# Kernel optimization log

Measured on AMD Instinct MI355X. Metric: run time of the kernel, lower is better.

The kernel has to match this reference:

```python
import jax, jax.numpy as jnp
import numpy as np

EPS_INTERP = 1e-8
EPS_BN = 1e-5


def _bn_relu(x, gamma, beta):
    # x: [B, C, N]; training-mode BatchNorm1d over (B, N) with biased variance
    mean = jnp.mean(x, axis=(0, 2), keepdims=True)
    var = jnp.mean((x - mean) ** 2, axis=(0, 2), keepdims=True)
    xn = (x - mean) / jnp.sqrt(var + EPS_BN)
    return jax.nn.relu(xn * gamma[None, :, None] + beta[None, :, None])


def setup_inputs() -> dict:
    key = jax.random.key(0)
    ks = jax.random.split(key, 8)
    B, N, S, D = 16, 4096, 1024, 128
    return {
        "xyz1": jax.random.normal(ks[0], (B, 3, N), jnp.float32),
        "xyz2": jax.random.normal(ks[1], (B, 3, S), jnp.float32),
        "points1": jax.random.normal(ks[2], (B, D, N), jnp.float32),
        "points2": jax.random.normal(ks[3], (B, D, S), jnp.float32),
        "w0": jax.random.normal(ks[4], (256, 512), jnp.float32) * 0.04,
        "b0": jax.random.normal(ks[5], (256,), jnp.float32) * 0.01,
        "gamma0": jnp.ones((256,), jnp.float32),
        "beta0": jnp.zeros((256,), jnp.float32),
        "w1": jax.random.normal(ks[6], (128, 256), jnp.float32) * 0.06,
        "b1": jax.random.normal(ks[7], (128,), jnp.float32) * 0.01,
        "gamma1": jnp.ones((128,), jnp.float32),
        "beta1": jnp.zeros((128,), jnp.float32),
    }


def reference(xyz1, xyz2, points1, points2, w0, b0, gamma0, beta0, w1, b1, gamma1, beta1):
    # to [B, N, C] layouts
    x1 = jnp.transpose(xyz1, (0, 2, 1))   # [B, N, 3]
    x2 = jnp.transpose(xyz2, (0, 2, 1))   # [B, S, 3]
    p2 = jnp.transpose(points2, (0, 2, 1))  # [B, S, D]
    B, N, _ = x1.shape

    # squared pairwise distances [B, N, S]
    dists = (jnp.sum(x1 ** 2, -1)[:, :, None]
             + jnp.sum(x2 ** 2, -1)[:, None, :]
             - 2.0 * jnp.einsum('bnc,bsc->bns', x1, x2))

    # 3 nearest neighbors (ascending distance)
    neg_d, idx = jax.lax.top_k(-dists, 3)   # idx: [B, N, 3]
    d3 = -neg_d
    recip = 1.0 / (d3 + EPS_INTERP)
    weight = recip / jnp.sum(recip, axis=2, keepdims=True)  # [B, N, 3]

    # gather neighbor features: [B, N, 3, D]
    gathered = jax.vmap(lambda p, i: p[i])(p2, idx)
    # NOTE: this repo flattens the 3 weighted neighbors (no sum) -> [B, N, 3*D]
    interp = (gathered * weight[..., None]).reshape(B, N, -1)

    new_pts = jnp.concatenate([jnp.transpose(points1, (0, 2, 1)), interp], axis=-1)  # [B, N, 512]
    x = jnp.transpose(new_pts, (0, 2, 1))  # [B, 512, N]

    x = _bn_relu(jnp.einsum('oc,bcn->bon', w0, x) + b0[None, :, None], gamma0, beta0)
    x = _bn_relu(jnp.einsum('oc,bcn->bon', w1, x) + b1[None, :, None], gamma1, beta1)
    return x
```

## Files before the change

kernel.cpp:

```cpp
#include <hip/hip_runtime.h>
#include <stdint.h>

typedef unsigned short ushort_t;
typedef __attribute__((ext_vector_type(8))) __bf16 bf16x8;
typedef __attribute__((ext_vector_type(4))) float f32x4;

__device__ __forceinline__ float b2f(ushort_t u) {
    unsigned v = ((unsigned)u) << 16;
    float f;
    __builtin_memcpy(&f, &v, 4);
    return f;
}

__device__ __forceinline__ ushort_t f2b(float f) {
    __bf16 h = (__bf16)f;
    return __builtin_bit_cast(ushort_t, h);
}

__device__ __forceinline__ void gl_lds16(const void* g, void* l) {
    __builtin_amdgcn_global_load_lds((const __attribute__((address_space(1))) void*)g,
                                     (__attribute__((address_space(3))) void*)l, 16, 0, 0);
}

__global__ __launch_bounds__(256) void k_pre(const float* __restrict__ w0, ushort_t* __restrict__ w0b,
                                             const float* __restrict__ w1, ushort_t* __restrict__ w1b,
                                             const float* __restrict__ xyz2, float4* __restrict__ sdat,
                                             const float* __restrict__ points2, ushort_t* __restrict__ p2t,
                                             float* __restrict__ zb) {
    int bid = blockIdx.x;
    int t = threadIdx.x;
    if (bid < 512) {
        int i = bid * 256 + t;
        w0b[i] = f2b(w0[i]);
    } else if (bid < 640) {
        int i = (bid - 512) * 256 + t;
        w1b[i] = f2b(w1[i]);
    } else if (bid < 704) {
        int bb = bid - 640;
        int b = bb & 15, by = bb >> 4;
        int s = by * 256 + t;
        const float* x2 = xyz2 + (size_t)b * 3 * 1024;
        float x = x2[s], y = x2[1024 + s], z = x2[2048 + s];
        float4 v;
        v.x = x; v.y = y; v.z = z;
        v.w = __fadd_rn(__fadd_rn(__fmul_rn(x, x), __fmul_rn(y, y)), __fmul_rn(z, z));
        sdat[(size_t)b * 1024 + s] = v;
    } else if (bid < 960) {
        int bb = bid - 704;
        int b = bb & 15, sy = bb >> 4;
        int s = sy * 64 + (t & 63);
        int g = t >> 6;
        const float* src = points2 + (size_t)b * 128 * 1024 + s;
        ushort_t* dst = p2t + ((size_t)b * 1024 + s) * 128;
#pragma unroll
        for (int i = 0; i < 4; ++i) {
            int cp = i * 4 + g;
            ushort_t tmp[8];
#pragma unroll
            for (int k = 0; k < 8; ++k) tmp[k] = f2b(src[(size_t)(cp * 8 + k) * 1024]);
            *(uint4*)(dst + cp * 8) = *(const uint4*)tmp;
        }
    } else {
        for (int i = t; i < 6144; i += 256) zb[i] = 0.f;
    }
}

__global__ __launch_bounds__(256) void k_interp(const float* __restrict__ xyz1,
                                                const float4* __restrict__ sdat,
                                                const float* __restrict__ points1,
                                                const ushort_t* __restrict__ p2t,
                                                ushort_t* __restrict__ X) {
    int b = blockIdx.x;
    int n0 = blockIdx.y * 32;
    int t = threadIdx.x;
    int tq = t & 31;
    int slice = t >> 5;
    int wave = t >> 6, lane = t & 63;

    __shared__ __align__(16) char sbuf[16384];
    float4* sP = (float4*)sbuf;
    int*   sidx = (int*)sbuf;
    float* sw   = (float*)(sbuf + 384);
    __shared__ float sD[768];
    __shared__ int   sI[768];

    {
        const float4* src = sdat + (size_t)b * 1024;
#pragma unroll
        for (int c = 0; c < 4; ++c) {
            int p = wave * 256 + c * 64 + lane;
            gl_lds16(src + p, sbuf + p * 16);
        }
    }

    int n = n0 + tq;
    float x = xyz1[((size_t)b * 3 + 0) * 4096 + n];
    float y = xyz1[((size_t)b * 3 + 1) * 4096 + n];
    float z = xyz1[((size_t)b * 3 + 2) * 4096 + n];
    float s1 = __fadd_rn(__fadd_rn(__fmul_rn(x, x), __fmul_rn(y, y)), __fmul_rn(z, z));

    __syncthreads();

    const float* p1base = points1 + (size_t)b * 128 * 4096 + n0 + tq;
    float p1v[16];
#pragma unroll
    for (int i = 0; i < 2; ++i)
#pragma unroll
        for (int k = 0; k < 8; ++k)
            p1v[i * 8 + k] = p1base[(size_t)(((i * 8 + slice) * 8) + k) * 4096];

    float d0 = 1e30f, d1 = 1e30f, d2 = 1e30f;
    int i0 = 0, i1 = 0, i2 = 0;
    int sbeg = slice * 128;
    const float4* sdL = sP + sbeg;
#pragma unroll 8
    for (int s = 0; s < 128; ++s) {
        float4 v = sdL[s];
        float dot = fmaf(z, v.z, fmaf(y, v.y, __fmul_rn(x, v.x)));
        float d = __fadd_rn(fmaf(-2.0f, dot, s1), v.w);
        int si = sbeg + s;
        bool c0 = d < d0, c1 = d < d1, c2 = d < d2;
        i2 = c1 ? i1 : (c2 ? si : i2);
        i1 = c0 ? i0 : (c1 ? si : i1);
        i0 = c0 ? si : i0;
        d2 = fminf(fmaxf(d, d1), d2);
        d1 = fminf(fmaxf(d, d0), d1);
        d0 = fminf(d, d0);
    }
    sD[t * 3 + 0] = d0; sD[t * 3 + 1] = d1; sD[t * 3 + 2] = d2;
    sI[t * 3 + 0] = i0; sI[t * 3 + 1] = i1; sI[t * 3 + 2] = i2;

    {
        ushort_t* dstbase = X + (size_t)(b * 4096 + n0 + tq) * 512;
#pragma unroll
        for (int i = 0; i < 2; ++i) {
            int piece = i * 8 + slice;
            ushort_t tmp[8];
#pragma unroll
            for (int k = 0; k < 8; ++k) tmp[k] = f2b(p1v[i * 8 + k]);
            *(uint4*)(dstbase + piece * 8) = *(const uint4*)tmp;
        }
    }
    __syncthreads();

    if (t < 32) {
        int sel0 = -1, sel1 = -1;
        float seld[3]; int seli[3];
#pragma unroll
        for (int r = 0; r < 3; ++r) {
            float bd = 1e38f; int bi = 1 << 30;
            for (int k = 0; k < 24; ++k) {
                int s3 = (k * 0xAAAB) >> 17;
                int rank = k - s3 * 3;
                int base = (s3 * 32 + t) * 3 + rank;
                float cd = sD[base];
                int ci = sI[base];
                bool excl = (ci == sel0) | (ci == sel1);
                bool better = (!excl) & ((cd < bd) | ((cd == bd) & (ci < bi)));
                if (better) { bd = cd; bi = ci; }
            }
            seld[r] = bd; seli[r] = bi;
            if (r == 0) sel0 = bi; else if (r == 1) sel1 = bi;
        }
        float r0 = 1.0f / (seld[0] + 1e-8f);
        float r1 = 1.0f / (seld[1] + 1e-8f);
        float r2 = 1.0f / (seld[2] + 1e-8f);
        float rs = r0 + r1 + r2;
        sw[t * 3 + 0] = r0 / rs; sw[t * 3 + 1] = r1 / rs; sw[t * 3 + 2] = r2 / rs;
        sidx[t * 3 + 0] = seli[0]; sidx[t * 3 + 1] = seli[1]; sidx[t * 3 + 2] = seli[2];
    }
    __syncthreads();

#pragma unroll
    for (int i = 0; i < 6; ++i) {
        int idx = i * 256 + t;
        int q = idx / 48;
        int rem = idx - q * 48;
        int r = rem >> 4;
        int piece = rem & 15;
        int si = sidx[q * 3 + r] & 1023;
        float wt = sw[q * 3 + r];
        const ushort_t* src = p2t + ((size_t)b * 1024 + si) * 128 + piece * 8;
        uint4 raw = *(const uint4*)src;
        ushort_t* e = (ushort_t*)&raw;
        ushort_t outv[8];
#pragma unroll
        for (int k = 0; k < 8; ++k) outv[k] = f2b(wt * b2f(e[k]));
        ushort_t* dst = X + (size_t)(b * 4096 + n0 + q) * 512 + 128 + r * 128 + piece * 8;
        *(uint4*)dst = *(const uint4*)outv;
    }
}

__global__ __launch_bounds__(512, 4) void k_gemm(const ushort_t* __restrict__ A,
                                                 const ushort_t* __restrict__ Bt,
                                                 const float* __restrict__ bias,
                                                 ushort_t* __restrict__ Y,
                                                 float* __restrict__ gs,
                                                 float* __restrict__ gq,
                                                 int Mtot, int K) {
    __shared__ __align__(16) char smem[51200];
    ushort_t* As = (ushort_t*)smem;
    ushort_t* Bs = (ushort_t*)(smem + 32768);
    ushort_t* sY = (ushort_t*)smem;
    float* red_s = (float*)(smem + 49152);
    float* red_q = red_s + 256;

    int t = threadIdx.x;
    int j0 = blockIdx.x * 128;
    int wave = t >> 6, lane = t & 63;
    int wm = wave >> 1, wn = wave & 1;
    int l16 = lane & 15, quad = lane >> 4;

    if (t < 256) { red_s[t] = 0.f; red_q[t] = 0.f; }

    f32x4 acc[4][4] = {};

    int nk = K >> 6;
    for (int kt = 0; kt < nk; ++kt) {
#pragma unroll
        for (int c = 0; c < 4; ++c) {
            int idx = c * 512 + t;
            int row = idx >> 3, kc = idx & 7;
            gl_lds16(A + (size_t)row * K + kt * 64 + kc * 8, As + idx * 8);
        }
#pragma unroll
        for (int c = 0; c < 2; ++c) {
            int idx = c * 512 + t;
            int row = idx >> 3, kc = idx & 7;
            gl_lds16(Bt + (size_t)(j0 + row) * K + kt * 64 + kc * 8, Bs + idx * 8);
        }
        __syncthreads();

#pragma unroll
        for (int kk = 0; kk < 2; ++kk) {
            bf16x8 af[4], bfr[4];
#pragma unroll
            for (int mi = 0; mi < 4; ++mi)
                af[mi] = *(const bf16x8*)(As + (wm * 64 + mi * 16 + l16) * 64 + kk * 32 + quad * 8);
#pragma unroll
            for (int ni = 0; ni < 4; ++ni)
                bfr[ni] = *(const bf16x8*)(Bs + (wn * 64 + ni * 16 + l16) * 64 + kk * 32 + quad * 8);
#pragma unroll
            for (int mi = 0; mi < 4; ++mi)
#pragma unroll
                for (int ni = 0; ni < 4; ++ni)
                    acc[mi][ni] = __builtin_amdgcn_mfma_f32_16x16x32_bf16(af[mi], bfr[ni], acc[mi][ni], 0, 0, 0);
        }
        __syncthreads();
    }

#pragma unroll
    for (int h = 0; h < 2; ++h) {
        if ((wm >> 1) == h) {
#pragma unroll
            for (int mi = 0; mi < 4; ++mi) {
                int obase = wm * 64 + mi * 16 + quad * 4;
                int ocol = obase - h * 128;
                float bv[4];
#pragma unroll
                for (int r = 0; r < 4; ++r) bv[r] = bias[obase + r];
                float sr[4] = {0.f, 0.f, 0.f, 0.f}, qr[4] = {0.f, 0.f, 0.f, 0.f};
#pragma unroll
                for (int ni = 0; ni < 4; ++ni) {
                    int j_local = wn * 64 + ni * 16 + l16;
                    ushort4 pk;
                    float v0 = acc[mi][ni][0] + bv[0];
                    float v1 = acc[mi][ni][1] + bv[1];
                    float v2 = acc[mi][ni][2] + bv[2];
                    float v3 = acc[mi][ni][3] + bv[3];
                    pk.x = f2b(v0); pk.y = f2b(v1); pk.z = f2b(v2); pk.w = f2b(v3);
                    sr[0] += v0; qr[0] += v0 * v0;
                    sr[1] += v1; qr[1] += v1 * v1;
                    sr[2] += v2; qr[2] += v2 * v2;
                    sr[3] += v3; qr[3] += v3 * v3;
                    *(ushort4*)(sY + j_local * 136 + ocol) = pk;
                }
#pragma unroll
                for (int r = 0; r < 4; ++r) {
                    float s = sr[r], q = qr[r];
                    s += __shfl_xor(s, 1); s += __shfl_xor(s, 2);
                    s += __shfl_xor(s, 4); s += __shfl_xor(s, 8);
                    q += __shfl_xor(q, 1); q += __shfl_xor(q, 2);
                    q += __shfl_xor(q, 4); q += __shfl_xor(q, 8);
                    if (l16 == 0) {
                        atomicAdd(&red_s[obase + r], s);
                        atomicAdd(&red_q[obase + r], q);
                    }
                }
            }
        }
        __syncthreads();
#pragma unroll
        for (int rep = 0; rep < 4; ++rep) {
            int idx = rep * 512 + t;
            int jl = idx >> 4;
            int o8 = idx & 15;
            uint4 vv = *(const uint4*)(sY + jl * 136 + o8 * 8);
            *(uint4*)(Y + (size_t)(j0 + jl) * Mtot + h * 128 + o8 * 8) = vv;
        }
        __syncthreads();
    }
    if (t < 256) {
        int cp = blockIdx.x & 7;
        atomicAdd(&gs[cp * 256 + t], red_s[t]);
        atomicAdd(&gq[cp * 256 + t], red_q[t]);
    }
}

__global__ __launch_bounds__(256) void k_gemmf(const ushort_t* __restrict__ A,
                                               const ushort_t* __restrict__ Y0,
                                               const float* __restrict__ bias,
                                               const float* __restrict__ gamma0,
                                               const float* __restrict__ beta0,
                                               const float* __restrict__ gs0,
                                               const float* __restrict__ gq0,
                                               ushort_t* __restrict__ Y,
                                               float* __restrict__ gs1,
                                               float* __restrict__ gq1,
                                               int Mtot, int K) {
    __shared__ __align__(16) char smem[35840];
    ushort_t* As = (ushort_t*)smem;
    ushort_t* Bs = (ushort_t*)(smem + 16384);
    float* sa = (float*)(smem + 32768);
    float* sb = (float*)(smem + 33792);
    ushort_t* sY = (ushort_t*)smem;
    float* red_s = (float*)(smem + 34816);
    float* red_q = red_s + 128;

    int t = threadIdx.x;
    int m0 = blockIdx.x * 128;
    int j0 = blockIdx.y * 128;
    int wave = t >> 6, lane = t & 63;
    int wm = wave >> 1, wn = wave & 1;
    int l16 = lane & 15, quad = lane >> 4;

    {
        float s = 0.f, q = 0.f;
#pragma unroll
        for (int k = 0; k < 8; ++k) { s += gs0[k * 256 + t]; q += gq0[k * 256 + t]; }
        float mean = s * (1.0f / 65536.0f);
        float var = q * (1.0f / 65536.0f) - mean * mean;
        float sc = gamma0[t] / sqrtf(var + 1e-5f);
        sa[t] = sc;
        sb[t] = beta0[t] - mean * sc;
    }
    if (t < 128) { red_s[t] = 0.f; red_q[t] = 0.f; }
    __syncthreads();

    f32x4 acc[4][4] = {};

    int nk = K >> 6;
    for (int kt = 0; kt < nk; ++kt) {
#pragma unroll
        for (int c = 0; c < 4; ++c) {
            int idx = c * 256 + t;
            int row = idx >> 3, kc = idx & 7;
            gl_lds16(A + (size_t)(m0 + row) * K + kt * 64 + kc * 8, As + idx * 8);
        }
#pragma unroll
        for (int c = 0; c < 4; ++c) {
            int idx = c * 256 + t;
            int row = idx >> 3, kc = idx & 7;
            int cbase = kt * 64 + kc * 8;
            uint4 raw = *(const uint4*)(Y0 + (size_t)(j0 + row) * K + cbase);
            ushort_t* e = (ushort_t*)&raw;
            ushort_t outv[8];
#pragma unroll
            for (int k = 0; k < 8; ++k) {
                float v = fmaxf(sa[cbase + k] * b2f(e[k]) + sb[cbase + k], 0.f);
                outv[k] = f2b(v);
            }
            *(uint4*)(Bs + idx * 8) = *(const uint4*)outv;
        }
        __syncthreads();

#pragma unroll
        for (int kk = 0; kk < 2; ++kk) {
            bf16x8 af[4], bfr[4];
#pragma unroll
            for (int mi = 0; mi < 4; ++mi)
                af[mi] = *(const bf16x8*)(As + (wm * 64 + mi * 16 + l16) * 64 + kk * 32 + quad * 8);
#pragma unroll
            for (int ni = 0; ni < 4; ++ni)
                bfr[ni] = *(const bf16x8*)(Bs + (wn * 64 + ni * 16 + l16) * 64 + kk * 32 + quad * 8);
#pragma unroll
            for (int mi = 0; mi < 4; ++mi)
#pragma unroll
                for (int ni = 0; ni < 4; ++ni)
                    acc[mi][ni] = __builtin_amdgcn_mfma_f32_16x16x32_bf16(af[mi], bfr[ni], acc[mi][ni], 0, 0, 0);
        }
        __syncthreads();
    }

#pragma unroll
    for (int mi = 0; mi < 4; ++mi) {
        int obase = wm * 64 + mi * 16 + quad * 4;
        float bv[4];
#pragma unroll
        for (int r = 0; r < 4; ++r) bv[r] = bias[m0 + obase + r];
        float sr[4] = {0.f, 0.f, 0.f, 0.f}, qr[4] = {0.f, 0.f, 0.f, 0.f};
#pragma unroll
        for (int ni = 0; ni < 4; ++ni) {
            int j_local = wn * 64 + ni * 16 + l16;
            ushort4 pk;
            float v0 = acc[mi][ni][0] + bv[0];
            float v1 = acc[mi][ni][1] + bv[1];
            float v2 = acc[mi][ni][2] + bv[2];
            float v3 = acc[mi][ni][3] + bv[3];
            pk.x = f2b(v0); pk.y = f2b(v1); pk.z = f2b(v2); pk.w = f2b(v3);
            sr[0] += v0; qr[0] += v0 * v0;
            sr[1] += v1; qr[1] += v1 * v1;
            sr[2] += v2; qr[2] += v2 * v2;
            sr[3] += v3; qr[3] += v3 * v3;
            *(ushort4*)(sY + j_local * 136 + obase) = pk;
        }
#pragma unroll
        for (int r = 0; r < 4; ++r) {
            float s = sr[r], q = qr[r];
            s += __shfl_xor(s, 1); s += __shfl_xor(s, 2);
            s += __shfl_xor(s, 4); s += __shfl_xor(s, 8);
            q += __shfl_xor(q, 1); q += __shfl_xor(q, 2);
            q += __shfl_xor(q, 4); q += __shfl_xor(q, 8);
            if (l16 == 0) {
                atomicAdd(&red_s[obase + r], s);
                atomicAdd(&red_q[obase + r], q);
            }
        }
    }
    __syncthreads();

#pragma unroll
    for (int rep = 0; rep < 8; ++rep) {
        int idx = rep * 256 + t;
        int jl = idx >> 4;
        int o8 = idx & 15;
        uint4 vv = *(const uint4*)(sY + jl * 136 + o8 * 8);
        *(uint4*)(Y + (size_t)(j0 + jl) * Mtot + m0 + o8 * 8) = vv;
    }
    if (t < 128) {
        int cp = blockIdx.y & 7;
        atomicAdd(&gs1[cp * 128 + m0 + t], red_s[t]);
        atomicAdd(&gq1[cp * 128 + m0 + t], red_q[t]);
    }
}

__global__ __launch_bounds__(256) void k_out(const ushort_t* __restrict__ Y1,
                                             const float* __restrict__ gs1,
                                             const float* __restrict__ gq1,
                                             const float* __restrict__ gamma1,
                                             const float* __restrict__ beta1,
                                             float* __restrict__ out) {
    __shared__ float sa[128], sb[128];
    int t = threadIdx.x;
    if (t < 128) {
        float s = 0.f, q = 0.f;
#pragma unroll
        for (int k = 0; k < 8; ++k) { s += gs1[k * 128 + t]; q += gq1[k * 128 + t]; }
        float mean = s * (1.0f / 65536.0f);
        float var = q * (1.0f / 65536.0f) - mean * mean;
        float sc = gamma1[t] / sqrtf(var + 1e-5f);
        sa[t] = sc;
        sb[t] = beta1[t] - mean * sc;
    }
    __syncthreads();
    int b = blockIdx.x;
    int nl = t & 127;
    int half = t >> 7;
    int n = blockIdx.y * 128 + nl;
    const uint4* src = (const uint4*)(Y1 + (size_t)(b * 4096 + n) * 128);
    float* dst = out + (size_t)b * 128 * 4096 + n;
    uint4 raw[8];
#pragma unroll
    for (int p = 0; p < 8; ++p) raw[p] = src[half * 8 + p];
    const ushort_t* e = (const ushort_t*)raw;
#pragma unroll
    for (int c = 0; c < 64; ++c) {
        int ch = half * 64 + c;
        float v = b2f(e[c]);
        v = fmaxf(sa[ch] * v + sb[ch], 0.f);
        dst[(size_t)ch * 4096] = v;
    }
}

extern "C" void kernel_launch(void* const* d_in, const int* in_sizes, int n_in,
                              void* d_out, int out_size, void* d_ws, size_t ws_size,
                              hipStream_t stream) {
    const float* xyz1    = (const float*)d_in[0];
    const float* xyz2    = (const float*)d_in[1];
    const float* points1 = (const float*)d_in[2];
    const float* points2 = (const float*)d_in[3];
    const float* w0      = (const float*)d_in[4];
    const float* b0      = (const float*)d_in[5];
    const float* gamma0  = (const float*)d_in[6];
    const float* beta0   = (const float*)d_in[7];
    const float* w1      = (const float*)d_in[8];
    const float* b1      = (const float*)d_in[9];
    const float* gamma1  = (const float*)d_in[10];
    const float* beta1   = (const float*)d_in[11];
    float* out = (float*)d_out;

    char* ws = (char*)d_ws;
    const size_t OFF_X    = 0;
    const size_t OFF_Y0   = 67108864;
    const size_t OFF_Y1   = 100663296;
    const size_t OFF_P2T  = 117440512;
    const size_t OFF_W0B  = 121634816;
    const size_t OFF_W1B  = 121896960;
    const size_t OFF_SDAT = 121965568;
    const size_t OFF_AB   = 122227712;

    ushort_t* X    = (ushort_t*)(ws + OFF_X);
    ushort_t* Y0   = (ushort_t*)(ws + OFF_Y0);
    ushort_t* Y1   = (ushort_t*)(ws + OFF_Y1);
    ushort_t* p2t  = (ushort_t*)(ws + OFF_P2T);
    ushort_t* w0b  = (ushort_t*)(ws + OFF_W0B);
    ushort_t* w1b  = (ushort_t*)(ws + OFF_W1B);
    float4* sdat   = (float4*)(ws + OFF_SDAT);
    float* ab      = (float*)(ws + OFF_AB);
    float* gs0 = ab;               float* gq0 = ab + 2048;
    float* gs1 = ab + 4096;        float* gq1 = ab + 5120;

    k_pre<<<961, 256, 0, stream>>>(w0, w0b, w1, w1b, xyz2, sdat, points2, p2t, ab);
    k_interp<<<dim3(16, 128), 256, 0, stream>>>(xyz1, sdat, points1, p2t, X);
    k_gemm<<<512, 512, 0, stream>>>(w0b, X, b0, Y0, gs0, gq0, 256, 512);
    k_gemmf<<<dim3(1, 512), 256, 0, stream>>>(w1b, Y0, b1, gamma0, beta0, gs0, gq0, Y1, gs1, gq1, 128, 256);
    k_out<<<dim3(16, 32), 256, 0, stream>>>(Y1, gs1, gq1, gamma1, beta1, out);
}
```

Measured before the change: 204.2 us.

## Fuse interpolation and first GEMM to keep concatenated features in LDS

The interpolation kernel now builds the 32x512 concatenated bf16 feature tile in shared memory with an XOR swizzle instead of writing it to a global X buffer. It then runs the first 256x512 projection on that tile directly with MFMA, reading the weights from global memory, and writes Y0 plus the BN partial sums. This drops the 64 MB X write and its re-read by a separate GEMM kernel, and one launch. In exchange each block reloads the full weight matrix from global/L2 with small 32-column tiles, shared memory doubles, and the per-block global atomics to the BN stats increase.

```diff
diff --git a/kernel.cpp b/kernel.cpp
--- a/kernel.cpp
+++ b/kernel.cpp
@@ -65,24 +65,31 @@
     }
 }
 
-__global__ __launch_bounds__(256) void k_interp(const float* __restrict__ xyz1,
-                                                const float4* __restrict__ sdat,
-                                                const float* __restrict__ points1,
-                                                const ushort_t* __restrict__ p2t,
-                                                ushort_t* __restrict__ X) {
+__global__ __launch_bounds__(256, 4) void k_fused(const float* __restrict__ xyz1,
+                                                  const float4* __restrict__ sdat,
+                                                  const float* __restrict__ points1,
+                                                  const ushort_t* __restrict__ p2t,
+                                                  const ushort_t* __restrict__ W,
+                                                  const float* __restrict__ bias,
+                                                  ushort_t* __restrict__ Y0,
+                                                  float* __restrict__ gs,
+                                                  float* __restrict__ gq) {
     int b = blockIdx.x;
     int n0 = blockIdx.y * 32;
     int t = threadIdx.x;
     int tq = t & 31;
     int slice = t >> 5;
     int wave = t >> 6, lane = t & 63;
-
-    __shared__ __align__(16) char sbuf[16384];
+    int l16 = lane & 15, quad = lane >> 4;
+
+    __shared__ __align__(16) char sbuf[32768];
     float4* sP = (float4*)sbuf;
-    int*   sidx = (int*)sbuf;
-    float* sw   = (float*)(sbuf + 384);
-    __shared__ float sD[768];
-    __shared__ int   sI[768];
+    float* sD  = (float*)(sbuf + 16384);
+    int*   sI  = (int*)(sbuf + 19456);
+    ushort_t* Xs  = (ushort_t*)sbuf;
+    ushort_t* sYl = (ushort_t*)sbuf;
+    __shared__ int   sidx[96];
+    __shared__ float sw[96];
 
     {
         const float4* src = sdat + (size_t)b * 1024;
@@ -129,18 +136,6 @@
     }
     sD[t * 3 + 0] = d0; sD[t * 3 + 1] = d1; sD[t * 3 + 2] = d2;
     sI[t * 3 + 0] = i0; sI[t * 3 + 1] = i1; sI[t * 3 + 2] = i2;
-
-    {
-        ushort_t* dstbase = X + (size_t)(b * 4096 + n0 + tq) * 512;
-#pragma unroll
-        for (int i = 0; i < 2; ++i) {
-            int piece = i * 8 + slice;
-            ushort_t tmp[8];
-#pragma unroll
-            for (int k = 0; k < 8; ++k) tmp[k] = f2b(p1v[i * 8 + k]);
-            *(uint4*)(dstbase + piece * 8) = *(const uint4*)tmp;
-        }
-    }
     __syncthreads();
 
     if (t < 32) {
@@ -171,6 +166,16 @@
     }
     __syncthreads();
 
+    {
+#pragma unroll
+        for (int i = 0; i < 2; ++i) {
+            int piece = i * 8 + slice;
+            ushort_t tmp[8];
+#pragma unroll
+            for (int k = 0; k < 8; ++k) tmp[k] = f2b(p1v[i * 8 + k]);
+            *(uint4*)(Xs + tq * 512 + ((piece ^ (tq & 7)) * 8)) = *(const uint4*)tmp;
+        }
+    }
 #pragma unroll
     for (int i = 0; i < 6; ++i) {
         int idx = i * 256 + t;
@@ -180,130 +185,79 @@
         int piece = rem & 15;
         int si = sidx[q * 3 + r] & 1023;
         float wt = sw[q * 3 + r];
-        const ushort_t* src = p2t + ((size_t)b * 1024 + si) * 128 + piece * 8;
-        uint4 raw = *(const uint4*)src;
+        uint4 raw = *(const uint4*)(p2t + ((size_t)b * 1024 + si) * 128 + piece * 8);
         ushort_t* e = (ushort_t*)&raw;
         ushort_t outv[8];
 #pragma unroll
         for (int k = 0; k < 8; ++k) outv[k] = f2b(wt * b2f(e[k]));
-        ushort_t* dst = X + (size_t)(b * 4096 + n0 + q) * 512 + 128 + r * 128 + piece * 8;
-        *(uint4*)dst = *(const uint4*)outv;
-    }
-}
-
-__global__ __launch_bounds__(512, 4) void k_gemm(const ushort_t* __restrict__ A,
-                                                 const ushort_t* __restrict__ Bt,
-                                                 const float* __restrict__ bias,
-                                                 ushort_t* __restrict__ Y,
-                                                 float* __restrict__ gs,
-                                                 float* __restrict__ gq,
-                                                 int Mtot, int K) {
-    __shared__ __align__(16) char smem[51200];
-    ushort_t* As = (ushort_t*)smem;
-    ushort_t* Bs = (ushort_t*)(smem + 32768);
-    ushort_t* sY = (ushort_t*)smem;
-    float* red_s = (float*)(smem + 49152);
-    float* red_q = red_s + 256;
-
-    int t = threadIdx.x;
-    int j0 = blockIdx.x * 128;
-    int wave = t >> 6, lane = t & 63;
-    int wm = wave >> 1, wn = wave & 1;
-    int l16 = lane & 15, quad = lane >> 4;
-
-    if (t < 256) { red_s[t] = 0.f; red_q[t] = 0.f; }
-
-    f32x4 acc[4][4] = {};
-
-    int nk = K >> 6;
-    for (int kt = 0; kt < nk; ++kt) {
-#pragma unroll
-        for (int c = 0; c < 4; ++c) {
-            int idx = c * 512 + t;
-            int row = idx >> 3, kc = idx & 7;
-            gl_lds16(A + (size_t)row * K + kt * 64 + kc * 8, As + idx * 8);
-        }
-#pragma unroll
-        for (int c = 0; c < 2; ++c) {
-            int idx = c * 512 + t;
-            int row = idx >> 3, kc = idx & 7;
-            gl_lds16(Bt + (size_t)(j0 + row) * K + kt * 64 + kc * 8, Bs + idx * 8);
-        }
-        __syncthreads();
-
-#pragma unroll
-        for (int kk = 0; kk < 2; ++kk) {
-            bf16x8 af[4], bfr[4];
-#pragma unroll
-            for (int mi = 0; mi < 4; ++mi)
-                af[mi] = *(const bf16x8*)(As + (wm * 64 + mi * 16 + l16) * 64 + kk * 32 + quad * 8);
-#pragma unroll
-            for (int ni = 0; ni < 4; ++ni)
-                bfr[ni] = *(const bf16x8*)(Bs + (wn * 64 + ni * 16 + l16) * 64 + kk * 32 + quad * 8);
-#pragma unroll
-            for (int mi = 0; mi < 4; ++mi)
-#pragma unroll
-                for (int ni = 0; ni < 4; ++ni)
-                    acc[mi][ni] = __builtin_amdgcn_mfma_f32_16x16x32_bf16(af[mi], bfr[ni], acc[mi][ni], 0, 0, 0);
-        }
-        __syncthreads();
-    }
-
-#pragma unroll
-    for (int h = 0; h < 2; ++h) {
-        if ((wm >> 1) == h) {
-#pragma unroll
-            for (int mi = 0; mi < 4; ++mi) {
-                int obase = wm * 64 + mi * 16 + quad * 4;
-                int ocol = obase - h * 128;
-                float bv[4];
-#pragma unroll
-                for (int r = 0; r < 4; ++r) bv[r] = bias[obase + r];
-                float sr[4] = {0.f, 0.f, 0.f, 0.f}, qr[4] = {0.f, 0.f, 0.f, 0.f};
-#pragma unroll
-                for (int ni = 0; ni < 4; ++ni) {
-                    int j_local = wn * 64 + ni * 16 + l16;
-                    ushort4 pk;
-                    float v0 = acc[mi][ni][0] + bv[0];
-                    float v1 = acc[mi][ni][1] + bv[1];
-                    float v2 = acc[mi][ni][2] + bv[2];
-                    float v3 = acc[mi][ni][3] + bv[3];
-                    pk.x = f2b(v0); pk.y = f2b(v1); pk.z = f2b(v2); pk.w = f2b(v3);
-                    sr[0] += v0; qr[0] += v0 * v0;
-                    sr[1] += v1; qr[1] += v1 * v1;
-                    sr[2] += v2; qr[2] += v2 * v2;
-                    sr[3] += v3; qr[3] += v3 * v3;
-                    *(ushort4*)(sY + j_local * 136 + ocol) = pk;
-                }
-#pragma unroll
-                for (int r = 0; r < 4; ++r) {
-                    float s = sr[r], q = qr[r];
-                    s += __shfl_xor(s, 1); s += __shfl_xor(s, 2);
-                    s += __shfl_xor(s, 4); s += __shfl_xor(s, 8);
-                    q += __shfl_xor(q, 1); q += __shfl_xor(q, 2);
-                    q += __shfl_xor(q, 4); q += __shfl_xor(q, 8);
-                    if (l16 == 0) {
-                        atomicAdd(&red_s[obase + r], s);
-                        atomicAdd(&red_q[obase + r], q);
-                    }
-                }
+        int chunk = 16 + r * 16 + piece;
+        *(uint4*)(Xs + q * 512 + ((chunk ^ (q & 7)) * 8)) = *(const uint4*)outv;
+    }
+    __syncthreads();
+
+    f32x4 acc[4][2] = {};
+    int sw7 = l16 & 7;
+#pragma unroll
+    for (int ks = 0; ks < 16; ++ks) {
+        bf16x8 af[4], bfr[2];
+#pragma unroll
+        for (int mi = 0; mi < 4; ++mi)
+            af[mi] = *(const bf16x8*)(W + (size_t)(wave * 64 + mi * 16 + l16) * 512 + ks * 32 + quad * 8);
+#pragma unroll
+        for (int ni = 0; ni < 2; ++ni)
+            bfr[ni] = *(const bf16x8*)(Xs + (ni * 16 + l16) * 512 + (((ks * 4 + quad) ^ sw7) * 8));
+#pragma unroll
+        for (int mi = 0; mi < 4; ++mi)
+#pragma unroll
+            for (int ni = 0; ni < 2; ++ni)
+                acc[mi][ni] = __builtin_amdgcn_mfma_f32_16x16x32_bf16(af[mi], bfr[ni], acc[mi][ni], 0, 0, 0);
+    }
+    __syncthreads();
+
+    int cp = blockIdx.y & 7;
+#pragma unroll
+    for (int mi = 0; mi < 4; ++mi) {
+        int obase = wave * 64 + mi * 16 + quad * 4;
+        float bv[4];
+#pragma unroll
+        for (int r = 0; r < 4; ++r) bv[r] = bias[obase + r];
+        float sr[4] = {0.f, 0.f, 0.f, 0.f}, qr[4] = {0.f, 0.f, 0.f, 0.f};
+#pragma unroll
+        for (int ni = 0; ni < 2; ++ni) {
+            int j_local = ni * 16 + l16;
+            ushort4 pk;
+            float v0 = acc[mi][ni][0] + bv[0];
+            float v1 = acc[mi][ni][1] + bv[1];
+            float v2 = acc[mi][ni][2] + bv[2];
+            float v3 = acc[mi][ni][3] + bv[3];
+            pk.x = f2b(v0); pk.y = f2b(v1); pk.z = f2b(v2); pk.w = f2b(v3);
+            sr[0] += v0; qr[0] += v0 * v0;
+            sr[1] += v1; qr[1] += v1 * v1;
+            sr[2] += v2; qr[2] += v2 * v2;
+            sr[3] += v3; qr[3] += v3 * v3;
+            *(ushort4*)(sYl + j_local * 256 + obase) = pk;
+        }
+#pragma unroll
+        for (int r = 0; r < 4; ++r) {
+            float s = sr[r], q = qr[r];
+            s += __shfl_xor(s, 1); s += __shfl_xor(s, 2);
+            s += __shfl_xor(s, 4); s += __shfl_xor(s, 8);
+            q += __shfl_xor(q, 1); q += __shfl_xor(q, 2);
+            q += __shfl_xor(q, 4); q += __shfl_xor(q, 8);
+            if (l16 == 0) {
+                atomicAdd(&gs[cp * 256 + obase + r], s);
+                atomicAdd(&gq[cp * 256 + obase + r], q);
             }
         }
-        __syncthreads();
-#pragma unroll
-        for (int rep = 0; rep < 4; ++rep) {
-            int idx = rep * 512 + t;
-            int jl = idx >> 4;
-            int o8 = idx & 15;
-            uint4 vv = *(const uint4*)(sY + jl * 136 + o8 * 8);
-            *(uint4*)(Y + (size_t)(j0 + jl) * Mtot + h * 128 + o8 * 8) = vv;
-        }
-        __syncthreads();
-    }
-    if (t < 256) {
-        int cp = blockIdx.x & 7;
-        atomicAdd(&gs[cp * 256 + t], red_s[t]);
-        atomicAdd(&gq[cp * 256 + t], red_q[t]);
+    }
+    __syncthreads();
+
+    {
+        uint4* dst = (uint4*)(Y0 + (size_t)(b * 4096 + n0) * 256);
+        const uint4* srcv = (const uint4*)sYl;
+#pragma unroll
+        for (int rep = 0; rep < 4; ++rep)
+            dst[rep * 256 + t] = srcv[rep * 256 + t];
     }
 }
 
@@ -500,7 +454,6 @@
     float* out = (float*)d_out;
 
     char* ws = (char*)d_ws;
-    const size_t OFF_X    = 0;
     const size_t OFF_Y0   = 67108864;
     const size_t OFF_Y1   = 100663296;
     const size_t OFF_P2T  = 117440512;
@@ -509,7 +462,6 @@
     const size_t OFF_SDAT = 121965568;
     const size_t OFF_AB   = 122227712;
 
-    ushort_t* X    = (ushort_t*)(ws + OFF_X);
     ushort_t* Y0   = (ushort_t*)(ws + OFF_Y0);
     ushort_t* Y1   = (ushort_t*)(ws + OFF_Y1);
     ushort_t* p2t  = (ushort_t*)(ws + OFF_P2T);
@@ -521,8 +473,7 @@
     float* gs1 = ab + 4096;        float* gq1 = ab + 5120;
 
     k_pre<<<961, 256, 0, stream>>>(w0, w0b, w1, w1b, xyz2, sdat, points2, p2t, ab);
-    k_interp<<<dim3(16, 128), 256, 0, stream>>>(xyz1, sdat, points1, p2t, X);
-    k_gemm<<<512, 512, 0, stream>>>(w0b, X, b0, Y0, gs0, gq0, 256, 512);
+    k_fused<<<dim3(16, 128), 256, 0, stream>>>(xyz1, sdat, points1, p2t, w0b, b0, Y0, gs0, gq0);
     k_gemmf<<<dim3(1, 512), 256, 0, stream>>>(w1b, Y0, b1, gamma0, beta0, gs0, gq0, Y1, gs1, gq1, 128, 256);
     k_out<<<dim3(16, 32), 256, 0, stream>>>(Y1, gs1, gq1, gamma1, beta1, out);
 }
```

New measurement: 217.9 us. 6.7% more time.
